# Performance work log

Hardware: AMD Instinct MI355X
Metric: run time of the kernel (lower is better)

The kernel has to match this reference:

```python
import jax, jax.numpy as jnp
from jax import lax
import numpy as np

INPUT_DIM = 1024; ENT_DIM = 256; KEY_DIM = 32; FUNC_DIM = 256; HID = 32
NUM_LAYERS = 1; UNIT_TYPE_DIM = 259; MAX_ENT = 64; B = 256; N = 512
NEG = 1e9

def _ln(x, g, b, eps=1e-5):
    m = x.mean(-1, keepdims=True)
    v = ((x - m) ** 2).mean(-1, keepdims=True)
    return (x - m) / jnp.sqrt(v + eps) * g + b

def setup_inputs() -> dict:
    key = jax.random.key(0)
    ks = jax.random.split(key, 16)
    def lin(k, i, o, s=0.02):
        return jax.random.normal(k, (i, o), jnp.float32) * s, jnp.zeros((o,), jnp.float32)
    p = {}
    p['key_fc_w'], p['key_fc_b'] = lin(ks[0], ENT_DIM, KEY_DIM)
    p['func_fc_w'], p['func_fc_b'] = lin(ks[1], UNIT_TYPE_DIM, FUNC_DIM)
    p['fc1_w'], p['fc1_b'] = lin(ks[2], INPUT_DIM, FUNC_DIM)
    p['fc2_w'], p['fc2_b'] = lin(ks[3], FUNC_DIM, KEY_DIM)
    p['embed_fc_w'], p['embed_fc_b'] = lin(ks[4], KEY_DIM, INPUT_DIM)
    p['lstm_wx'] = jax.random.normal(ks[5], (NUM_LAYERS, KEY_DIM, 4 * HID), jnp.float32) * 0.05
    p['lstm_wh'] = jax.random.normal(ks[6], (NUM_LAYERS, HID, 4 * HID), jnp.float32) * 0.05
    p['lstm_b'] = jnp.zeros((NUM_LAYERS, 4 * HID), jnp.float32)
    p['lstm_ln_gx'] = jnp.ones((NUM_LAYERS, 4 * HID), jnp.float32)
    p['lstm_ln_bx'] = jnp.zeros((NUM_LAYERS, 4 * HID), jnp.float32)
    p['lstm_ln_gh'] = jnp.ones((NUM_LAYERS, 4 * HID), jnp.float32)
    p['lstm_ln_bh'] = jnp.zeros((NUM_LAYERS, 4 * HID), jnp.float32)
    inp = {
        'embedding': jax.random.normal(ks[7], (B, INPUT_DIM), jnp.float32),
        'available_unit_type_mask': (jax.random.uniform(ks[8], (B, UNIT_TYPE_DIM)) < 0.5).astype(jnp.float32),
        'available_units_mask': jnp.ones((B, N), jnp.float32),
        'entity_embedding': jax.random.normal(ks[9], (B, N, ENT_DIM), jnp.float32),
        'temperature': jnp.float32(1.0),
    }
    inp.update(p)
    return inp

def reference(embedding, available_unit_type_mask, available_units_mask, entity_embedding,
              temperature, key_fc_w, key_fc_b, func_fc_w, func_fc_b, fc1_w, fc1_b,
              fc2_w, fc2_b, embed_fc_w, embed_fc_b, lstm_wx, lstm_wh, lstm_b,
              lstm_ln_gx, lstm_ln_bx, lstm_ln_gh, lstm_ln_bh):
    relu = jax.nn.relu
    # _get_key: [B,N,KEY] + end-flag row of zeros -> [B,N+1,KEY]
    key = entity_embedding @ key_fc_w + key_fc_b
    key = jnp.concatenate([key, jnp.zeros((B, 1, KEY_DIM), key.dtype)], axis=1)
    end_idx = N
    # _get_init_query
    func_embed = relu(available_unit_type_mask @ func_fc_w + func_fc_b)
    x0 = relu(embedding @ fc1_w + fc1_b)
    x0 = relu((x0 + func_embed) @ fc2_w + fc2_b)  # [B, KEY_DIM]
    mask0 = jnp.concatenate([available_units_mask, jnp.ones((B, 1), available_units_mask.dtype)], axis=1)

    h0 = jnp.zeros((NUM_LAYERS, B, HID), key.dtype)
    c0 = jnp.zeros((NUM_LAYERS, B, HID), key.dtype)
    units0 = jnp.zeros((B, N + 1), jnp.int32)
    done0 = jnp.zeros((B,), bool)
    rng0 = jax.random.key(42)

    def step(carry, _):
        x, h, c, mask, units, done, rng = carry
        xi = x
        hs, cs = [], []
        for l in range(NUM_LAYERS):  # LN-LSTM, gate order i,f,o,u (DI-engine)
            gate = (_ln(xi @ lstm_wx[l], lstm_ln_gx[l], lstm_ln_bx[l])
                    + _ln(h[l] @ lstm_wh[l], lstm_ln_gh[l], lstm_ln_bh[l]) + lstm_b[l])
            i_g, f_g, o_g, u_g = jnp.split(gate, 4, axis=-1)
            cl = jax.nn.sigmoid(f_g) * c[l] + jax.nn.sigmoid(i_g) * jnp.tanh(u_g)
            hl = jax.nn.sigmoid(o_g) * jnp.tanh(cl)
            hs.append(hl); cs.append(cl); xi = hl
        h_new = jnp.stack(hs); c_new = jnp.stack(cs)
        q = (xi[:, None, :] * key).mean(-1)          # [B, N+1] pointer scores
        q = q - (1.0 - mask) * NEG
        rng, sk = jax.random.split(rng)
        idx = jax.random.categorical(sk, q / temperature, axis=-1)  # [B]
        is_end = idx == end_idx
        active = jnp.logical_not(done)
        sel = active & jnp.logical_not(is_end)
        onehot = jax.nn.one_hot(idx, N + 1, dtype=mask.dtype)
        units = jnp.where(sel[:, None] & (onehot > 0.5), 1, units)
        mask = jnp.where(sel[:, None], mask * (1.0 - onehot), mask)
        done = done | (active & is_end)
        return (xi, h_new, c_new, mask, units, done, rng), (q, active)

    carry, (logits, valid) = lax.scan(step, (x0, h0, c0, mask0, units0, done0, rng0), None, length=MAX_ENT)
    units = carry[4]
    emb_sel = (units[..., None].astype(key.dtype) * key).mean(axis=1)  # [B, KEY_DIM]
    emb_sel = emb_sel @ embed_fc_w + embed_fc_b
    return logits, valid, units, embedding + emb_sel
```

## Files before the change

### kernel.cpp

```cpp
#include <hip/hip_runtime.h>
#include <stdint.h>
#include <stddef.h>

#define JAX_PARTITIONABLE 1

#define B_   256
#define N_   512
#define NP_  513
#define KROW 516
#define T_   64
#define NEGC 1e9f

__host__ __device__ __forceinline__ void tf2x32(uint32_t k0, uint32_t k1,
    uint32_t x0, uint32_t x1, uint32_t& o0, uint32_t& o1) {
  const uint32_t k2 = k0 ^ k1 ^ 0x1BD11BDAu;
#define TFR(r) { x0 += x1; x1 = (x1 << (r)) | (x1 >> (32 - (r))); x1 ^= x0; }
  x0 += k0; x1 += k1;
  TFR(13) TFR(15) TFR(26) TFR(6)
  x0 += k1; x1 += k2 + 1u;
  TFR(17) TFR(29) TFR(16) TFR(24)
  x0 += k2; x1 += k0 + 2u;
  TFR(13) TFR(15) TFR(26) TFR(6)
  x0 += k0; x1 += k1 + 3u;
  TFR(17) TFR(29) TFR(16) TFR(24)
  x0 += k1; x1 += k2 + 4u;
  TFR(13) TFR(15) TFR(26) TFR(6)
  x0 += k2; x1 += k0 + 5u;
#undef TFR
  o0 = x0; o1 = x1;
}

struct SkKeys { uint32_t k[128]; };

static SkKeys compute_chain() {
  SkKeys s;
  uint32_t r0 = 0u, r1 = 42u;
  for (int t = 0; t < 64; ++t) {
#if JAX_PARTITIONABLE
    uint32_t a0, a1, b0, b1;
    tf2x32(r0, r1, 0u, 0u, a0, a1);
    tf2x32(r0, r1, 0u, 1u, b0, b1);
    s.k[2*t] = b0; s.k[2*t+1] = b1;
    r0 = a0; r1 = a1;
#else
    uint32_t p0, p1, q0, q1;
    tf2x32(r0, r1, 0u, 2u, p0, p1);
    tf2x32(r0, r1, 1u, 3u, q0, q1);
    s.k[2*t] = p1; s.k[2*t+1] = q1;
    r0 = p0; r1 = q0;
#endif
  }
  return s;
}

__device__ __forceinline__ float gumbel_draw(uint32_t k0, uint32_t k1, int b, int n) {
  uint32_t bits;
#if JAX_PARTITIONABLE
  uint32_t j = (uint32_t)(b * NP_ + n);
  uint32_t o0, o1; tf2x32(k0, k1, 0u, j, o0, o1);
  bits = o0 ^ o1;
#else
  int j = b * NP_ + n;
  uint32_t o0, o1;
  if (j < 65664) { tf2x32(k0, k1, (uint32_t)j, (uint32_t)(j + 65664), o0, o1); bits = o0; }
  else           { tf2x32(k0, k1, (uint32_t)(j - 65664), (uint32_t)j, o0, o1); bits = o1; }
#endif
  float f = __uint_as_float((bits >> 9) | 0x3F800000u) - 1.0f;
  const float TINY = 1.17549435e-38f;
  float u = fmaxf(TINY, f + TINY);
  return -logf(-logf(u));
}

__device__ __forceinline__ float sigm(float x) {
  return 0.5f + 0.5f * tanhf(0.5f * x);
}

__device__ __forceinline__ void bar_lds() {
  asm volatile("s_waitcnt lgkmcnt(0)\n\ts_barrier" ::: "memory");
}

#define WS_KEY 0
#define WS_X0  (B_ * 32 * KROW)

__global__ void __launch_bounds__(256)
pre_kernel(const float* __restrict__ ent, const float* __restrict__ key_w,
           const float* __restrict__ key_b,
           const float* __restrict__ emb, const float* __restrict__ fc1_w,
           const float* __restrict__ fc1_b,
           const float* __restrict__ autm, const float* __restrict__ func_w,
           const float* __restrict__ func_b,
           const float* __restrict__ fc2_w, const float* __restrict__ fc2_b,
           float* __restrict__ ws)
{
  __shared__ __align__(16) float smAll[16384];
  const int tid = threadIdx.x;

  if (blockIdx.x < 1024) {
    float* smA = smAll;
    float* smW = smAll + 8192;
    const int blk = blockIdx.x;
    const int R0  = blk * 128;
    const int b   = R0 >> 9;
    const int nb  = R0 & 511;
    const int rg  = tid >> 3;
    const int cg  = tid & 7;

    for (int i = tid; i < 2048; i += 256)
      ((float4*)smW)[i] = ((const float4*)key_w)[i];

    float acc[4][4];
    #pragma unroll
    for (int i = 0; i < 4; ++i)
      #pragma unroll
      for (int j = 0; j < 4; ++j) acc[i][j] = 0.f;

    const int row  = tid >> 1;
    const int half = tid & 1;

    for (int kc = 0; kc < 4; ++kc) {
      const float4* src = (const float4*)(ent + ((size_t)(R0 + row)) * 256 + kc * 64 + half * 32);
      float4 vv[8];
      #pragma unroll
      for (int r = 0; r < 8; ++r) vv[r] = src[r];
      #pragma unroll
      for (int r = 0; r < 8; ++r) {
        const int kl = half * 32 + r * 4;
        smA[(kl + 0) * 128 + row] = vv[r].x;
        smA[(kl + 1) * 128 + row] = vv[r].y;
        smA[(kl + 2) * 128 + row] = vv[r].z;
        smA[(kl + 3) * 128 + row] = vv[r].w;
      }
      __syncthreads();
      #pragma unroll 4
      for (int k = 0; k < 64; ++k) {
        float4 av = *(const float4*)&smA[k * 128 + rg * 4];
        float4 bv = *(const float4*)&smW[(kc * 64 + k) * 32 + cg * 4];
        float ar[4] = {av.x, av.y, av.z, av.w};
        float br[4] = {bv.x, bv.y, bv.z, bv.w};
        #pragma unroll
        for (int i = 0; i < 4; ++i)
          #pragma unroll
          for (int j = 0; j < 4; ++j) acc[i][j] += ar[i] * br[j];
      }
      __syncthreads();
    }
    float4 bb = *(const float4*)&key_b[cg * 4];
    float bbr[4] = {bb.x, bb.y, bb.z, bb.w};
    #pragma unroll
    for (int j = 0; j < 4; ++j) {
      const int c = cg * 4 + j;
      float* dst = ws + WS_KEY + ((size_t)(b * 32 + c)) * KROW + nb + rg * 4;
      #pragma unroll
      for (int i = 0; i < 4; ++i) dst[i] = acc[i][j] + bbr[j];
    }
  } else {
    float* smX = smAll;
    const int b = blockIdx.x - 1024;
    const int j = tid;
    {
      float a = 0.f;
      const float* e = emb + (size_t)b * 1024;
      #pragma unroll 8
      for (int k = 0; k < 1024; ++k) a += e[k] * fc1_w[k * 256 + j];
      a = fmaxf(a + fc1_b[j], 0.f);
      float f = 0.f;
      const float* m = autm + (size_t)b * 259;
      for (int k = 0; k < 259; ++k) f += m[k] * func_w[k * 256 + j];
      f = fmaxf(f + func_b[j], 0.f);
      smX[j] = a + f;
    }
    __syncthreads();
    if (j < 32) {
      float s = 0.f;
      #pragma unroll 8
      for (int m = 0; m < 256; ++m) s += smX[m] * fc2_w[m * 32 + j];
      ws[WS_X0 + b * 32 + j] = fmaxf(s + fc2_b[j], 0.f);
    }
  }
}

#define OFF_KEY   0
#define OFF_MASK  16512
#define OFF_UNITS 17028
#define OFF_GUM   17544
#define OFF_HS    18060
#define OFF_RV    18092
#define OFF_RI    18094
#define OFF_ES    18096
#define OFF_PART  18128
#define LDS_FLOATS 18640

__global__ void __launch_bounds__(512)
suh_kernel(const float* __restrict__ ws_key_x0,
           const float* __restrict__ aum, const float* __restrict__ temp_p,
           const float* __restrict__ emb,
           const float* __restrict__ emb_w, const float* __restrict__ emb_b,
           const float* __restrict__ wx, const float* __restrict__ wh,
           const float* __restrict__ lstm_bb,
           const float* __restrict__ ln_gx, const float* __restrict__ ln_bx,
           const float* __restrict__ ln_gh, const float* __restrict__ ln_bh,
           float* __restrict__ out_logits, float* __restrict__ out_valid,
           float* __restrict__ out_units, float* __restrict__ out_final,
           SkKeys sk)
{
  extern __shared__ __align__(16) float sm[];
  int* smi = (int*)sm;
  const int b   = blockIdx.x;
  const int tid = threadIdx.x;
  const int l6  = tid & 63;

  {
    const float4* kv = (const float4*)(ws_key_x0 + WS_KEY + (size_t)b * (32 * KROW));
    for (int i = tid; i < (32 * KROW) / 4; i += 512) ((float4*)sm)[i] = kv[i];
  }
  {
    const float* am = aum + (size_t)b * N_;
    for (int n = tid; n < NP_; n += 512) {
      sm[OFF_MASK + n]  = (n < N_) ? am[n] : 1.0f;
      sm[OFF_UNITS + n] = 0.f;
    }
  }
  __syncthreads();
  if (tid < 32) sm[OFF_KEY + tid * KROW + N_] = 0.f;
  __syncthreads();

  const float temp = temp_p[0];

  float wxr0[32], wxr1[32], whr0[32], whr1[32];
  #pragma unroll
  for (int k = 0; k < 32; ++k) {
    wxr0[k] = wx[k * 128 + l6];
    wxr1[k] = wx[k * 128 + 64 + l6];
    whr0[k] = wh[k * 128 + l6];
    whr1[k] = wh[k * 128 + 64 + l6];
  }
  float gxg0=0.f, gxg1=0.f, gxb0=0.f, gxb1=0.f, lb0=0.f, lb1=0.f;
  float ghg0=0.f, ghg1=0.f, ghb0=0.f, ghb1=0.f;
  if (tid < 64) {
    gxg0 = ln_gx[tid]; gxg1 = ln_gx[tid + 64];
    gxb0 = ln_bx[tid]; gxb1 = ln_bx[tid + 64];
    ghg0 = ln_gh[tid]; ghg1 = ln_gh[tid + 64];
    ghb0 = ln_bh[tid]; ghb1 = ln_bh[tid + 64];
    lb0  = lstm_bb[tid]; lb1 = lstm_bb[tid + 64];
  }

  float creg = 0.f;
  int done_reg = 0;

  for (int t = 0; t < T_; ++t) {
    const uint32_t kk0 = sk.k[2 * t], kk1 = sk.k[2 * t + 1];

    if (tid < 64) {
      float xfrag[32];
      if (t == 0) {
        const float* x0g = ws_key_x0 + WS_X0 + b * 32;
        #pragma unroll
        for (int r = 0; r < 8; ++r) {
          float4 v = *(const float4*)(x0g + r * 4);
          xfrag[r*4] = v.x; xfrag[r*4+1] = v.y; xfrag[r*4+2] = v.z; xfrag[r*4+3] = v.w;
        }
      } else {
        #pragma unroll
        for (int r = 0; r < 8; ++r) {
          float4 v = *(const float4*)&sm[OFF_HS + r * 4];
          xfrag[r*4] = v.x; xfrag[r*4+1] = v.y; xfrag[r*4+2] = v.z; xfrag[r*4+3] = v.w;
        }
      }
      float a0 = 0.f, a1 = 0.f, b0 = 0.f, b1 = 0.f;
      #pragma unroll
      for (int k = 0; k < 32; ++k) {
        a0 += xfrag[k] * wxr0[k];
        a1 += xfrag[k] * wxr1[k];
      }
      if (t > 0) {
        #pragma unroll
        for (int k = 0; k < 32; ++k) {
          b0 += xfrag[k] * whr0[k];
          b1 += xfrag[k] * whr1[k];
        }
      }
      float sx = a0 + a1, sh = b0 + b1;
      for (int off = 32; off; off >>= 1) {
        sx += __shfl_down(sx, off);
        sh += __shfl_down(sh, off);
      }
      float mx  = __shfl(sx, 0) * (1.0f / 128.0f);
      float mhh = __shfl(sh, 0) * (1.0f / 128.0f);
      float dx0 = a0 - mx, dx1 = a1 - mx;
      float dh0 = b0 - mhh, dh1 = b1 - mhh;
      float ssx = dx0 * dx0 + dx1 * dx1;
      float ssh = dh0 * dh0 + dh1 * dh1;
      for (int off = 32; off; off >>= 1) {
        ssx += __shfl_down(ssx, off);
        ssh += __shfl_down(ssh, off);
      }
      float vx = __shfl(ssx, 0) * (1.0f / 128.0f);
      float vh = __shfl(ssh, 0) * (1.0f / 128.0f);
      float rx = 1.0f / sqrtf(vx + 1e-5f);
      float rh = 1.0f / sqrtf(vh + 1e-5f);
      float lnx0 = dx0 * rx * gxg0 + gxb0;
      float lnx1 = dx1 * rx * gxg1 + gxb1;
      float lnh0 = dh0 * rh * ghg0 + ghb0;
      float lnh1 = dh1 * rh * ghg1 + ghb1;
      float g0 = lnx0 + lnh0 + lb0;
      float g1 = lnx1 + lnh1 + lb1;
      float fq = __shfl(g0, tid + 32);
      float uq = __shfl(g1, tid + 32);
      if (tid < 32) {
        float cN = sigm(fq) * creg + sigm(g0) * tanhf(uq);
        float hN = sigm(g1) * tanhf(cN);
        creg = cN;
        sm[OFF_HS + tid] = hN;
      }
    } else {
      const int n = tid - 64;
      sm[OFF_GUM + n] = gumbel_draw(kk0, kk1, b, n);
      if (tid < 129) sm[OFF_GUM + 448 + n] = gumbel_draw(kk0, kk1, b, 448 + n);
      if (tid == 511 && t > 0) {
        float r0v = sm[OFF_RV], r1v = sm[OFF_RV + 1];
        int   r0i = smi[OFF_RI], r1i = smi[OFF_RI + 1];
        float bvv; int bii;
        if (r1v > r0v || (r1v == r0v && r1i < r0i)) { bvv = r1v; bii = r1i; }
        else                                        { bvv = r0v; bii = r0i; }
        (void)bvv;
        const int active = !done_reg;
        const int is_end = (bii == N_);
        out_valid[(size_t)(t - 1) * B_ + b] = active ? 1.0f : 0.0f;
        if (active && !is_end) { sm[OFF_UNITS + bii] = 1.0f; sm[OFF_MASK + bii] = 0.0f; }
        if (active && is_end) done_reg = 1;
      }
    }
    bar_lds();

    if (tid < 128) {
      const int g = tid;
      float4 h4[8];
      #pragma unroll
      for (int r = 0; r < 8; ++r) h4[r] = *(const float4*)&sm[OFF_HS + r * 4];
      float hr[32] = {h4[0].x,h4[0].y,h4[0].z,h4[0].w, h4[1].x,h4[1].y,h4[1].z,h4[1].w,
                      h4[2].x,h4[2].y,h4[2].z,h4[2].w, h4[3].x,h4[3].y,h4[3].z,h4[3].w,
                      h4[4].x,h4[4].y,h4[4].z,h4[4].w, h4[5].x,h4[5].y,h4[5].z,h4[5].w,
                      h4[6].x,h4[6].y,h4[6].z,h4[6].w, h4[7].x,h4[7].y,h4[7].z,h4[7].w};
      float ac0 = 0.f, ac1 = 0.f, ac2 = 0.f, ac3 = 0.f;
      #pragma unroll
      for (int k = 0; k < 32; ++k) {
        float4 kv = *(const float4*)&sm[OFF_KEY + k * KROW + g * 4];
        float hk = hr[k];
        ac0 += hk * kv.x; ac1 += hk * kv.y; ac2 += hk * kv.z; ac3 += hk * kv.w;
      }
      float4 mv = *(const float4*)&sm[OFF_MASK + g * 4];
      float4 gv = *(const float4*)&sm[OFF_GUM + g * 4];
      float q0 = ac0 * (1.0f/32.0f) - (1.0f - mv.x) * NEGC;
      float q1 = ac1 * (1.0f/32.0f) - (1.0f - mv.y) * NEGC;
      float q2 = ac2 * (1.0f/32.0f) - (1.0f - mv.z) * NEGC;
      float q3 = ac3 * (1.0f/32.0f) - (1.0f - mv.w) * NEGC;
      float* lrow = out_logits + ((size_t)t * B_ + b) * NP_;
      lrow[g*4    ] = q0; lrow[g*4 + 1] = q1;
      lrow[g*4 + 2] = q2; lrow[g*4 + 3] = q3;
      float v0 = q0 / temp + gv.x;
      float v1 = q1 / temp + gv.y;
      float v2 = q2 / temp + gv.z;
      float v3 = q3 / temp + gv.w;
      float bv = v0; int bi = g*4;
      if (v1 > bv) { bv = v1; bi = g*4 + 1; }
      if (v2 > bv) { bv = v2; bi = g*4 + 2; }
      if (v3 > bv) { bv = v3; bi = g*4 + 3; }
      if (g == 0) {
        float q = -(1.0f - sm[OFF_MASK + N_]) * NEGC;
        lrow[N_] = q;
        float v = q / temp + sm[OFF_GUM + N_];
        if (v > bv) { bv = v; bi = N_; }
      }
      for (int off = 32; off; off >>= 1) {
        float ov = __shfl_down(bv, off);
        int   oi = __shfl_down(bi, off);
        if (ov > bv || (ov == bv && oi < bi)) { bv = ov; bi = oi; }
      }
      if ((tid & 63) == 0) { sm[OFF_RV + (tid >> 6)] = bv; smi[OFF_RI + (tid >> 6)] = bi; }
    }
    bar_lds();
  }

  if (tid == 511) {
    float r0v = sm[OFF_RV], r1v = sm[OFF_RV + 1];
    int   r0i = smi[OFF_RI], r1i = smi[OFF_RI + 1];
    float bvv; int bii;
    if (r1v > r0v || (r1v == r0v && r1i < r0i)) { bvv = r1v; bii = r1i; }
    else                                        { bvv = r0v; bii = r0i; }
    (void)bvv;
    const int active = !done_reg;
    const int is_end = (bii == N_);
    out_valid[(size_t)(T_ - 1) * B_ + b] = active ? 1.0f : 0.0f;
    if (active && !is_end) { sm[OFF_UNITS + bii] = 1.0f; sm[OFF_MASK + bii] = 0.0f; }
  }
  __syncthreads();

  {
    const int g = tid >> 5, cc = tid & 31;
    float p = 0.f;
    const int n0 = g * 32;
    for (int nn = 0; nn < 32; ++nn) {
      const int n = n0 + nn;
      p += sm[OFF_UNITS + n] * sm[OFF_KEY + cc * KROW + n];
    }
    if (g == 15) p += sm[OFF_UNITS + N_] * sm[OFF_KEY + cc * KROW + N_];
    sm[OFF_PART + g * 32 + cc] = p;
  }
  for (int n = tid; n < NP_; n += 512) out_units[(size_t)b * NP_ + n] = sm[OFF_UNITS + n];
  __syncthreads();
  if (tid < 32) {
    float s = 0.f;
    #pragma unroll
    for (int g = 0; g < 16; ++g) s += sm[OFF_PART + g * 32 + tid];
    sm[OFF_ES + tid] = s / 513.0f;
  }
  __syncthreads();
  {
    const float* e = emb + (size_t)b * 1024;
    for (int d = tid; d < 1024; d += 512) {
      float a = 0.f;
      #pragma unroll
      for (int k = 0; k < 32; ++k) a += sm[OFF_ES + k] * emb_w[k * 1024 + d];
      out_final[(size_t)b * 1024 + d] = e[d] + a + emb_b[d];
    }
  }
}

extern "C" void kernel_launch(void* const* d_in, const int* in_sizes, int n_in,
                              void* d_out, int out_size, void* d_ws, size_t ws_size,
                              hipStream_t stream) {
  (void)in_sizes; (void)n_in; (void)ws_size; (void)out_size;
  const float* emb    = (const float*)d_in[0];
  const float* autm   = (const float*)d_in[1];
  const float* aum    = (const float*)d_in[2];
  const float* ent    = (const float*)d_in[3];
  const float* temp   = (const float*)d_in[4];
  const float* key_w  = (const float*)d_in[5];
  const float* key_b  = (const float*)d_in[6];
  const float* func_w = (const float*)d_in[7];
  const float* func_b = (const float*)d_in[8];
  const float* fc1_w  = (const float*)d_in[9];
  const float* fc1_b  = (const float*)d_in[10];
  const float* fc2_w  = (const float*)d_in[11];
  const float* fc2_b  = (const float*)d_in[12];
  const float* emb_w  = (const float*)d_in[13];
  const float* emb_b  = (const float*)d_in[14];
  const float* wx     = (const float*)d_in[15];
  const float* wh     = (const float*)d_in[16];
  const float* lb     = (const float*)d_in[17];
  const float* gxg    = (const float*)d_in[18];
  const float* gxb    = (const float*)d_in[19];
  const float* ghg    = (const float*)d_in[20];
  const float* ghb    = (const float*)d_in[21];
  float* out = (float*)d_out;
  float* ws  = (float*)d_ws;

  const size_t OFF_V = (size_t)T_ * B_ * NP_;
  const size_t OFF_U = OFF_V + (size_t)T_ * B_;
  const size_t OFF_F = OFF_U + (size_t)B_ * NP_;

  SkKeys sk = compute_chain();

  pre_kernel<<<dim3(1280), dim3(256), 0, stream>>>(
      ent, key_w, key_b, emb, fc1_w, fc1_b, autm, func_w, func_b,
      fc2_w, fc2_b, ws);

  suh_kernel<<<dim3(B_), dim3(512), LDS_FLOATS * sizeof(float), stream>>>(
      ws, aum, temp, emb, emb_w, emb_b,
      wx, wh, lb, gxg, gxb, ghg, ghb,
      out, out + OFF_V, out + OFF_U, out + OFF_F, sk);
}
```

Measured before the change: 300.8 us.

## Decouple LSTM recurrence from pointer scoring and pipeline chunked score/Gumbel prep

The LSTM hidden state does not depend on the sampled index, so all 64 hidden states are now computed up front by one wavefront and stored in LDS. The pointer scores and Gumbel noise for chunks of 4 steps are then precomputed by the other waves, double-buffered, while a single wave runs the sequential argmax and mask update with the mask held in registers. This cuts the per-step block-wide barriers from two per step to one per chunk and moves the heavy dot products off the serial path. In exchange it uses much more LDS and adds a launch-bounds occupancy hint.

New measurement: 275.4 us. 8.4% less time.

```diff
diff --git a/kernel.cpp b/kernel.cpp
--- a/kernel.cpp
+++ b/kernel.cpp
@@ -9,6 +9,8 @@
 #define NP_  513
 #define KROW 516
 #define T_   64
+#define CS   4
+#define NCH  16
 #define NEGC 1e9f
 
 __host__ __device__ __forceinline__ void tf2x32(uint32_t k0, uint32_t k1,
@@ -180,17 +182,16 @@
 }
 
 #define OFF_KEY   0
-#define OFF_MASK  16512
-#define OFF_UNITS 17028
-#define OFF_GUM   17544
-#define OFF_HS    18060
-#define OFF_RV    18092
-#define OFF_RI    18094
-#define OFF_ES    18096
-#define OFF_PART  18128
-#define LDS_FLOATS 18640
-
-__global__ void __launch_bounds__(512)
+#define OFF_H     16512
+#define OFF_Q     18560
+#define OFF_G     22688
+#define OFF_UNITS 26816
+#define OFF_SK    27332
+#define OFF_ES    27460
+#define OFF_PART  27492
+#define LDS_FLOATS 28004
+
+__global__ void __launch_bounds__(512, 2)
 suh_kernel(const float* __restrict__ ws_key_x0,
            const float* __restrict__ aum, const float* __restrict__ temp_p,
            const float* __restrict__ emb,
@@ -207,65 +208,49 @@
   int* smi = (int*)sm;
   const int b   = blockIdx.x;
   const int tid = threadIdx.x;
-  const int l6  = tid & 63;
 
   {
     const float4* kv = (const float4*)(ws_key_x0 + WS_KEY + (size_t)b * (32 * KROW));
     for (int i = tid; i < (32 * KROW) / 4; i += 512) ((float4*)sm)[i] = kv[i];
   }
-  {
-    const float* am = aum + (size_t)b * N_;
-    for (int n = tid; n < NP_; n += 512) {
-      sm[OFF_MASK + n]  = (n < N_) ? am[n] : 1.0f;
-      sm[OFF_UNITS + n] = 0.f;
-    }
-  }
+  if (tid < 128) smi[OFF_SK + tid] = (int)sk.k[tid];
   __syncthreads();
   if (tid < 32) sm[OFF_KEY + tid * KROW + N_] = 0.f;
-  __syncthreads();
 
   const float temp = temp_p[0];
 
-  float wxr0[32], wxr1[32], whr0[32], whr1[32];
-  #pragma unroll
-  for (int k = 0; k < 32; ++k) {
-    wxr0[k] = wx[k * 128 + l6];
-    wxr1[k] = wx[k * 128 + 64 + l6];
-    whr0[k] = wh[k * 128 + l6];
-    whr1[k] = wh[k * 128 + 64 + l6];
-  }
-  float gxg0=0.f, gxg1=0.f, gxb0=0.f, gxb1=0.f, lb0=0.f, lb1=0.f;
-  float ghg0=0.f, ghg1=0.f, ghb0=0.f, ghb1=0.f;
+  float mreg[8], ureg[8];
+  float m512 = 1.0f;
+  int done_reg = 0;
+
   if (tid < 64) {
-    gxg0 = ln_gx[tid]; gxg1 = ln_gx[tid + 64];
-    gxb0 = ln_bx[tid]; gxb1 = ln_bx[tid + 64];
-    ghg0 = ln_gh[tid]; ghg1 = ln_gh[tid + 64];
-    ghb0 = ln_bh[tid]; ghb1 = ln_bh[tid + 64];
-    lb0  = lstm_bb[tid]; lb1 = lstm_bb[tid + 64];
-  }
-
-  float creg = 0.f;
-  int done_reg = 0;
-
-  for (int t = 0; t < T_; ++t) {
-    const uint32_t kk0 = sk.k[2 * t], kk1 = sk.k[2 * t + 1];
-
-    if (tid < 64) {
-      float xfrag[32];
-      if (t == 0) {
-        const float* x0g = ws_key_x0 + WS_X0 + b * 32;
-        #pragma unroll
-        for (int r = 0; r < 8; ++r) {
-          float4 v = *(const float4*)(x0g + r * 4);
-          xfrag[r*4] = v.x; xfrag[r*4+1] = v.y; xfrag[r*4+2] = v.z; xfrag[r*4+3] = v.w;
-        }
-      } else {
-        #pragma unroll
-        for (int r = 0; r < 8; ++r) {
-          float4 v = *(const float4*)&sm[OFF_HS + r * 4];
-          xfrag[r*4] = v.x; xfrag[r*4+1] = v.y; xfrag[r*4+2] = v.z; xfrag[r*4+3] = v.w;
-        }
-      }
+    float wxr0[32], wxr1[32], whr0[32], whr1[32];
+    #pragma unroll
+    for (int k = 0; k < 32; ++k) {
+      wxr0[k] = wx[k * 128 + tid];
+      wxr1[k] = wx[k * 128 + 64 + tid];
+      whr0[k] = wh[k * 128 + tid];
+      whr1[k] = wh[k * 128 + 64 + tid];
+    }
+    const float gxg0 = ln_gx[tid], gxg1 = ln_gx[tid + 64];
+    const float gxb0 = ln_bx[tid], gxb1 = ln_bx[tid + 64];
+    const float ghg0 = ln_gh[tid], ghg1 = ln_gh[tid + 64];
+    const float ghb0 = ln_bh[tid], ghb1 = ln_bh[tid + 64];
+    const float lb0  = lstm_bb[tid], lb1 = lstm_bb[tid + 64];
+
+    float xfrag[32];
+    {
+      const float* x0g = ws_key_x0 + WS_X0 + b * 32;
+      #pragma unroll
+      for (int r = 0; r < 8; ++r) {
+        float4 v = *(const float4*)(x0g + r * 4);
+        xfrag[r*4] = v.x; xfrag[r*4+1] = v.y; xfrag[r*4+2] = v.z; xfrag[r*4+3] = v.w;
+      }
+    }
+    float creg = 0.f;
+
+    #pragma unroll 1
+    for (int t = 0; t < T_; ++t) {
       float a0 = 0.f, a1 = 0.f, b0 = 0.f, b1 = 0.f;
       #pragma unroll
       for (int k = 0; k < 32; ++k) {
@@ -310,88 +295,118 @@
         float cN = sigm(fq) * creg + sigm(g0) * tanhf(uq);
         float hN = sigm(g1) * tanhf(cN);
         creg = cN;
-        sm[OFF_HS + tid] = hN;
-      }
-    } else {
-      const int n = tid - 64;
-      sm[OFF_GUM + n] = gumbel_draw(kk0, kk1, b, n);
-      if (tid < 129) sm[OFF_GUM + 448 + n] = gumbel_draw(kk0, kk1, b, 448 + n);
-      if (tid == 511 && t > 0) {
-        float r0v = sm[OFF_RV], r1v = sm[OFF_RV + 1];
-        int   r0i = smi[OFF_RI], r1i = smi[OFF_RI + 1];
-        float bvv; int bii;
-        if (r1v > r0v || (r1v == r0v && r1i < r0i)) { bvv = r1v; bii = r1i; }
-        else                                        { bvv = r0v; bii = r0i; }
-        (void)bvv;
+        sm[OFF_H + t * 32 + tid] = hN;
+      }
+      #pragma unroll
+      for (int r = 0; r < 8; ++r) {
+        float4 v = *(const float4*)&sm[OFF_H + t * 32 + r * 4];
+        xfrag[r*4] = v.x; xfrag[r*4+1] = v.y; xfrag[r*4+2] = v.z; xfrag[r*4+3] = v.w;
+      }
+    }
+  }
+  __syncthreads();
+
+  auto do_prep = [&](int cc, int pbuf) {
+    const int L = tid - 64;
+    const int qb = OFF_Q + pbuf * (CS * 516);
+    const int gb = OFF_G + pbuf * (CS * 516);
+    #pragma unroll 1
+    for (int pass = 0; pass < 2; ++pass) {
+      const int n = L + pass * 448;
+      if (pass == 0 || L < 65) {
+        float kreg[32];
+        #pragma unroll
+        for (int k = 0; k < 32; ++k) kreg[k] = sm[OFF_KEY + k * KROW + n];
+        #pragma unroll
+        for (int tl = 0; tl < CS; ++tl) {
+          float acc = 0.f;
+          #pragma unroll
+          for (int k = 0; k < 32; ++k) acc += sm[OFF_H + (cc * CS + tl) * 32 + k] * kreg[k];
+          sm[qb + tl * 516 + n] = acc * (1.0f / 32.0f);
+        }
+      }
+    }
+    #pragma unroll 1
+    for (int i = 0; i < (CS * 512 + 447) / 448; ++i) {
+      const int idx = i * 448 + L;
+      if (idx < CS * 512) {
+        const int tl = idx >> 9;
+        const int n  = idx & 511;
+        const int t  = cc * CS + tl;
+        sm[gb + tl * 516 + n] =
+            gumbel_draw((uint32_t)smi[OFF_SK + 2*t], (uint32_t)smi[OFF_SK + 2*t + 1], b, n);
+      }
+    }
+    if (L < CS) {
+      const int t = cc * CS + L;
+      sm[gb + L * 516 + N_] =
+          gumbel_draw((uint32_t)smi[OFF_SK + 2*t], (uint32_t)smi[OFF_SK + 2*t + 1], b, N_);
+    }
+  };
+
+  if (tid >= 64) {
+    do_prep(0, 0);
+  } else {
+    #pragma unroll
+    for (int j = 0; j < 8; ++j) {
+      const int n = tid + 64 * j;
+      mreg[j] = aum[(size_t)b * N_ + n];
+      ureg[j] = 0.f;
+    }
+  }
+  bar_lds();
+
+  for (int c = 0; c < NCH; ++c) {
+    const int pb = c & 1;
+    if (tid < 64) {
+      const int qbase = OFF_Q + pb * (CS * 516);
+      const int gbase = OFF_G + pb * (CS * 516);
+      #pragma unroll 1
+      for (int tl = 0; tl < CS; ++tl) {
+        const int t = c * CS + tl;
+        float* lrow = out_logits + ((size_t)t * B_ + b) * NP_;
+        float bv = 0.f; int bi = 0;
+        #pragma unroll
+        for (int j = 0; j < 8; ++j) {
+          const int n = tid + 64 * j;
+          float q = sm[qbase + tl * 516 + n] - (1.0f - mreg[j]) * NEGC;
+          lrow[n] = q;
+          float v = q / temp + sm[gbase + tl * 516 + n];
+          if (j == 0) { bv = v; bi = n; }
+          else if (v > bv) { bv = v; bi = n; }
+        }
+        if (tid == 0) {
+          float q = -(1.0f - m512) * NEGC;
+          lrow[N_] = q;
+          float v = q / temp + sm[gbase + tl * 516 + N_];
+          if (v > bv) { bv = v; bi = N_; }
+        }
+        for (int off = 32; off; off >>= 1) {
+          float ov = __shfl_down(bv, off);
+          int   oi = __shfl_down(bi, off);
+          if (ov > bv || (ov == bv && oi < bi)) { bv = ov; bi = oi; }
+        }
+        const int sel_i = __shfl(bi, 0);
         const int active = !done_reg;
-        const int is_end = (bii == N_);
-        out_valid[(size_t)(t - 1) * B_ + b] = active ? 1.0f : 0.0f;
-        if (active && !is_end) { sm[OFF_UNITS + bii] = 1.0f; sm[OFF_MASK + bii] = 0.0f; }
+        const int is_end = (sel_i == N_);
+        if (tid == 0) out_valid[(size_t)t * B_ + b] = active ? 1.0f : 0.0f;
+        if (active && !is_end) {
+          #pragma unroll
+          for (int j = 0; j < 8; ++j)
+            if (tid + 64 * j == sel_i) { mreg[j] = 0.0f; ureg[j] = 1.0f; }
+        }
         if (active && is_end) done_reg = 1;
       }
+    } else if (c + 1 < NCH) {
+      do_prep(c + 1, (c + 1) & 1);
     }
     bar_lds();
-
-    if (tid < 128) {
-      const int g = tid;
-      float4 h4[8];
-      #pragma unroll
-      for (int r = 0; r < 8; ++r) h4[r] = *(const float4*)&sm[OFF_HS + r * 4];
-      float hr[32] = {h4[0].x,h4[0].y,h4[0].z,h4[0].w, h4[1].x,h4[1].y,h4[1].z,h4[1].w,
-                      h4[2].x,h4[2].y,h4[2].z,h4[2].w, h4[3].x,h4[3].y,h4[3].z,h4[3].w,
-                      h4[4].x,h4[4].y,h4[4].z,h4[4].w, h4[5].x,h4[5].y,h4[5].z,h4[5].w,
-                      h4[6].x,h4[6].y,h4[6].z,h4[6].w, h4[7].x,h4[7].y,h4[7].z,h4[7].w};
-      float ac0 = 0.f, ac1 = 0.f, ac2 = 0.f, ac3 = 0.f;
-      #pragma unroll
-      for (int k = 0; k < 32; ++k) {
-        float4 kv = *(const float4*)&sm[OFF_KEY + k * KROW + g * 4];
-        float hk = hr[k];
-        ac0 += hk * kv.x; ac1 += hk * kv.y; ac2 += hk * kv.z; ac3 += hk * kv.w;
-      }
-      float4 mv = *(const float4*)&sm[OFF_MASK + g * 4];
-      float4 gv = *(const float4*)&sm[OFF_GUM + g * 4];
-      float q0 = ac0 * (1.0f/32.0f) - (1.0f - mv.x) * NEGC;
-      float q1 = ac1 * (1.0f/32.0f) - (1.0f - mv.y) * NEGC;
-      float q2 = ac2 * (1.0f/32.0f) - (1.0f - mv.z) * NEGC;
-      float q3 = ac3 * (1.0f/32.0f) - (1.0f - mv.w) * NEGC;
-      float* lrow = out_logits + ((size_t)t * B_ + b) * NP_;
-      lrow[g*4    ] = q0; lrow[g*4 + 1] = q1;
-      lrow[g*4 + 2] = q2; lrow[g*4 + 3] = q3;
-      float v0 = q0 / temp + gv.x;
-      float v1 = q1 / temp + gv.y;
-      float v2 = q2 / temp + gv.z;
-      float v3 = q3 / temp + gv.w;
-      float bv = v0; int bi = g*4;
-      if (v1 > bv) { bv = v1; bi = g*4 + 1; }
-      if (v2 > bv) { bv = v2; bi = g*4 + 2; }
-      if (v3 > bv) { bv = v3; bi = g*4 + 3; }
-      if (g == 0) {
-        float q = -(1.0f - sm[OFF_MASK + N_]) * NEGC;
-        lrow[N_] = q;
-        float v = q / temp + sm[OFF_GUM + N_];
-        if (v > bv) { bv = v; bi = N_; }
-      }
-      for (int off = 32; off; off >>= 1) {
-        float ov = __shfl_down(bv, off);
-        int   oi = __shfl_down(bi, off);
-        if (ov > bv || (ov == bv && oi < bi)) { bv = ov; bi = oi; }
-      }
-      if ((tid & 63) == 0) { sm[OFF_RV + (tid >> 6)] = bv; smi[OFF_RI + (tid >> 6)] = bi; }
-    }
-    bar_lds();
-  }
-
-  if (tid == 511) {
-    float r0v = sm[OFF_RV], r1v = sm[OFF_RV + 1];
-    int   r0i = smi[OFF_RI], r1i = smi[OFF_RI + 1];
-    float bvv; int bii;
-    if (r1v > r0v || (r1v == r0v && r1i < r0i)) { bvv = r1v; bii = r1i; }
-    else                                        { bvv = r0v; bii = r0i; }
-    (void)bvv;
-    const int active = !done_reg;
-    const int is_end = (bii == N_);
-    out_valid[(size_t)(T_ - 1) * B_ + b] = active ? 1.0f : 0.0f;
-    if (active && !is_end) { sm[OFF_UNITS + bii] = 1.0f; sm[OFF_MASK + bii] = 0.0f; }
+  }
+
+  if (tid < 64) {
+    #pragma unroll
+    for (int j = 0; j < 8; ++j) sm[OFF_UNITS + tid + 64 * j] = ureg[j];
+    if (tid == 0) sm[OFF_UNITS + N_] = 0.f;
   }
   __syncthreads();
 
```
